# Kernel tuning notes

Measured on AMD Instinct MI355X. Metric: run time of the kernel, lower is better.

Reference implementation:

```python
import jax, jax.numpy as jnp
import numpy as np

N_NODES = 100_000
N_EDGES = 1_600_000
IN_CH, HID, OUT_CH = 2, 64, 16


def setup_inputs() -> dict:
    key = jax.random.key(0)
    ks = jax.random.split(key, 6)
    x = jax.random.normal(ks[0], (N_NODES, IN_CH), dtype=jnp.float32)
    edge_index = jax.random.randint(ks[1], (2, N_EDGES), 0, N_NODES, dtype=jnp.int64)
    # Glorot-style init for GCN weights
    W1 = jax.random.normal(ks[2], (IN_CH, HID), dtype=jnp.float32) / np.sqrt(IN_CH)
    b1 = jnp.zeros((HID,), dtype=jnp.float32)
    W_mu = jax.random.normal(ks[3], (HID, OUT_CH), dtype=jnp.float32) / np.sqrt(HID)
    b_mu = jnp.zeros((OUT_CH,), dtype=jnp.float32)
    W_logstd = jax.random.normal(ks[4], (HID, OUT_CH), dtype=jnp.float32) / np.sqrt(HID)
    b_logstd = jnp.zeros((OUT_CH,), dtype=jnp.float32)
    return dict(x=x, edge_index=edge_index, W1=W1, b1=b1,
                W_mu=W_mu, b_mu=b_mu, W_logstd=W_logstd, b_logstd=b_logstd)


def _gcn_conv(x, W, b, src, dst, deg_inv_sqrt, n):
    h = x @ W                                   # [n, out]
    norm = deg_inv_sqrt[src] * deg_inv_sqrt[dst]  # [E]
    agg = jax.ops.segment_sum(norm[:, None] * h[src], dst, num_segments=n)
    agg = agg + (deg_inv_sqrt * deg_inv_sqrt)[:, None] * h  # self-loop term
    return agg + b


def reference(x, edge_index, W1, b1, W_mu, b_mu, W_logstd, b_logstd):
    n = x.shape[0]
    src, dst = edge_index[0], edge_index[1]
    # degree on A+I (self-loop contributes 1)
    deg = 1.0 + jax.ops.segment_sum(jnp.ones_like(src, dtype=x.dtype), dst, num_segments=n)
    dis = jax.lax.rsqrt(deg)
    h = jax.nn.relu(_gcn_conv(x, W1, b1, src, dst, dis, n))
    mu = _gcn_conv(h, W_mu, b_mu, src, dst, dis, n)
    logstd = _gcn_conv(h, W_logstd, b_logstd, src, dst, dis, n)
    return (mu, logstd)
```

## Files before the change

kernel.cpp:

```cpp
#include <hip/hip_runtime.h>
#include <hip/hip_fp16.h>
#include <math.h>


#define CH    4096
#define CAPB  4800

typedef float f32x4 __attribute__((ext_vector_type(4)));

__device__ __forceinline__ float2 cvt2(unsigned u) {
    __half2 h = *reinterpret_cast<__half2*>(&u);
    return __half22float2(h);
}

__device__ __forceinline__ int block_scan512(int* arr, int* tmp, int tid) {
    int v0 = arr[2 * tid], v1 = arr[2 * tid + 1];
    tmp[tid] = v0 + v1;
    __syncthreads();
    for (int off = 1; off < 256; off <<= 1) {
        int a = (tid >= off) ? tmp[tid - off] : 0;
        __syncthreads();
        tmp[tid] += a;
        __syncthreads();
    }
    int incl = tmp[tid];
    int base = incl - v0 - v1;
    arr[2 * tid] = base;
    arr[2 * tid + 1] = base + v0;
    int total = tmp[255];
    __syncthreads();
    return total;
}

__global__ void k_chunksort(const int* __restrict__ src, const int* __restrict__ dst,
                            unsigned* __restrict__ pairsc, unsigned* __restrict__ seg_t,
                            int E, int NC, int NBk) {
    __shared__ int hist[512];
    __shared__ int tmp[256];
    __shared__ int cur[392];
    __shared__ unsigned ebuf[CH];
    int c = blockIdx.x, tid = threadIdx.x;
    int e0 = c * CH;
    int n_e = min(CH, E - e0);

    hist[tid] = 0; hist[tid + 256] = 0;
    __syncthreads();
    for (int i = tid; i < n_e; i += 256) {
        int d = dst[e0 + i];
        atomicAdd(&hist[d >> 8], 1);
    }
    __syncthreads();
    int total = block_scan512(hist, tmp, tid);
    cur[tid] = hist[tid];
    if (tid < 136) cur[tid + 256] = hist[tid + 256];
    __syncthreads();
    for (int i = tid; i < n_e; i += 256) {
        int d = dst[e0 + i];
        int s = src[e0 + i];
        int slot = atomicAdd(&cur[d >> 8], 1);
        ebuf[slot] = ((unsigned)(d & 255) << 17) | (unsigned)s;
    }
    __syncthreads();
    for (int i = tid; i < n_e; i += 256)
        pairsc[(size_t)e0 + i] = ebuf[i];
    for (int b = tid; b < NBk; b += 256) {
        int base = hist[b];
        int next = (b + 1 < 512) ? hist[b + 1] : total;
        seg_t[(size_t)b * NC + c] = ((unsigned)(next - base) << 13) | (unsigned)base;
    }
}

__global__ void k_bucket256(const unsigned* __restrict__ pairsc,
                            const unsigned* __restrict__ seg_t,
                            const float* __restrict__ x,
                            uint2* __restrict__ rows2, float2* __restrict__ xd,
                            int* __restrict__ sorted_src, int NC, int N) {
    __shared__ int coff[512];
    __shared__ int tmp[256];
    __shared__ int hist[512];
    __shared__ int cur[256];
    __shared__ unsigned segs[392];
    __shared__ unsigned lbuf[CAPB];
    __shared__ unsigned sbuf[CAPB];
    int b = blockIdx.x, tid = threadIdx.x;

    for (int c = tid; c < NC; c += 256) segs[c] = seg_t[(size_t)b * NC + c];
    coff[tid] = 0; coff[tid + 256] = 0;
    __syncthreads();
    for (int c = tid; c < NC; c += 256) coff[c] = (int)(segs[c] >> 13);
    __syncthreads();
    int tot = block_scan512(coff, tmp, tid);

    for (int c = tid; c < NC; c += 256) {
        unsigned sg = segs[c];
        int len = (int)(sg >> 13);
        int base = (int)(sg & 0x1FFFu);
        int doff = coff[c];
        const unsigned* p = pairsc + (size_t)c * CH + base;
        for (int j = 0; j < len; ++j) lbuf[doff + j] = p[j];
    }
    hist[tid] = 0; hist[tid + 256] = 0;
    __syncthreads();
    for (int i = tid; i < tot; i += 256) atomicAdd(&hist[lbuf[i] >> 17], 1);
    __syncthreads();
    int deg = hist[tid];
    block_scan512(hist, tmp, tid);
    int excl = hist[tid];
    int n = (b << 8) + tid;
    int ebase = b * CAPB;
    if (n < N) {
        float di = rsqrtf(1.0f + (float)deg);
        rows2[n] = make_uint2((unsigned)(ebase + excl) | ((unsigned)deg << 21),
                              __float_as_uint(di));
        float2 xv = ((const float2*)x)[n];
        xd[n] = make_float2(di * xv.x, di * xv.y);
    }
    cur[tid] = excl;
    __syncthreads();
    for (int i = tid; i < tot; i += 256) {
        unsigned pr = lbuf[i];
        int slot = atomicAdd(&cur[pr >> 17], 1);
        sbuf[slot] = pr & 0x1FFFFu;
    }
    __syncthreads();
    for (int i = tid; i < tot; i += 256)
        sorted_src[ebase + i] = (int)sbuf[i];
}

__global__ void k_mlp(const float2* __restrict__ xd, const uint2* __restrict__ rows2,
                      const int* __restrict__ sorted_src,
                      const float* __restrict__ W1, const float* __restrict__ b1,
                      const float* __restrict__ W_mu, const float* __restrict__ W_logstd,
                      __half2* __restrict__ hml16, int N) {
    __shared__ float2 Wp[64 * 16];
    int tid = threadIdx.x;
    for (int t = tid; t < 1024; t += 256) {
        int k = t >> 4, c2 = t & 15;
        Wp[t] = make_float2(W_mu[k * 16 + c2], W_logstd[k * 16 + c2]);
    }
    int c2 = tid & 15;
    float w1a[4], w1b[4], bb[4];
#pragma unroll
    for (int j = 0; j < 4; ++j) {
        w1a[j] = W1[c2 + 16 * j];
        w1b[j] = W1[64 + c2 + 16 * j];
        bb[j]  = b1[c2 + 16 * j];
    }
    __syncthreads();
    int node = blockIdx.x * 16 + (tid >> 4);
    if (node >= N) return;
    uint2 r = rows2[node];
    int beg = (int)(r.x & 0x1FFFFFu);
    int end = beg + (int)(r.x >> 21);
    float di = __uint_as_float(r.y);
    float sx = 0.0f, sy = 0.0f;
    for (int e = beg + c2; e < end; e += 16) {
        int s = sorted_src[e];
        float2 u = xd[s];
        sx += u.x;
        sy += u.y;
    }
#pragma unroll
    for (int off = 8; off; off >>= 1) {
        sx += __shfl_xor(sx, off, 16);
        sy += __shfl_xor(sy, off, 16);
    }
    float2 xn = xd[node];
    float axx = di * (sx + xn.x);
    float axy = di * (sy + xn.y);
    float h[4];
#pragma unroll
    for (int j = 0; j < 4; ++j)
        h[j] = fmaxf(fmaf(axx, w1a[j], fmaf(axy, w1b[j], bb[j])), 0.0f);
    float2 a0 = make_float2(0.f, 0.f), a1 = a0, a2 = a0, a3 = a0;
#pragma unroll
    for (int kk = 0; kk < 16; ++kk) {
        float h0 = __shfl(h[0], kk, 16);
        float h1 = __shfl(h[1], kk, 16);
        float h2 = __shfl(h[2], kk, 16);
        float h3 = __shfl(h[3], kk, 16);
        float2 w0 = Wp[kk * 16 + c2];
        float2 w1 = Wp[(16 + kk) * 16 + c2];
        float2 w2 = Wp[(32 + kk) * 16 + c2];
        float2 w3 = Wp[(48 + kk) * 16 + c2];
        a0.x = fmaf(h0, w0.x, a0.x); a0.y = fmaf(h0, w0.y, a0.y);
        a1.x = fmaf(h1, w1.x, a1.x); a1.y = fmaf(h1, w1.y, a1.y);
        a2.x = fmaf(h2, w2.x, a2.x); a2.y = fmaf(h2, w2.y, a2.y);
        a3.x = fmaf(h3, w3.x, a3.x); a3.y = fmaf(h3, w3.y, a3.y);
    }
    float mu = di * ((a0.x + a1.x) + (a2.x + a3.x));
    float ls = di * ((a0.y + a1.y) + (a2.y + a3.y));
    hml16[(size_t)node * 16 + c2] = __floats2half2_rn(mu, ls);
}

__global__ void k_agg2(const __half2* __restrict__ hml16, const uint2* __restrict__ rows2,
                       const int* __restrict__ sorted_src,
                       const float* __restrict__ b_mu, const float* __restrict__ b_logstd,
                       float* __restrict__ out, int N) {
    int t = blockIdx.x * blockDim.x + threadIdx.x;
    int node = t >> 2, q = t & 3;
    if (node >= N) return;
    const uint4* h4 = (const uint4*)hml16;
    uint2 r = rows2[node];
    int beg = (int)(r.x & 0x1FFFFFu);
    int end = beg + (int)(r.x >> 21);
    float di = __uint_as_float(r.y);
    uint4 v = h4[(size_t)node * 4 + q];
    float2 a0 = cvt2(v.x), a1 = cvt2(v.y), a2 = cvt2(v.z), a3 = cvt2(v.w);
    for (int k = beg; k < end; ++k) {
        int s = sorted_src[k];
        uint4 u = h4[(size_t)s * 4 + q];
        float2 t0 = cvt2(u.x), t1 = cvt2(u.y), t2 = cvt2(u.z), t3 = cvt2(u.w);
        a0.x += t0.x; a0.y += t0.y; a1.x += t1.x; a1.y += t1.y;
        a2.x += t2.x; a2.y += t2.y; a3.x += t3.x; a3.y += t3.y;
    }
    float4 bm = *(const float4*)(b_mu + 4 * q);
    float4 bl = *(const float4*)(b_logstd + 4 * q);
    f32x4 mu = { fmaf(di, a0.x, bm.x), fmaf(di, a1.x, bm.y),
                 fmaf(di, a2.x, bm.z), fmaf(di, a3.x, bm.w) };
    f32x4 ls = { fmaf(di, a0.y, bl.x), fmaf(di, a1.y, bl.y),
                 fmaf(di, a2.y, bl.z), fmaf(di, a3.y, bl.w) };
    *(f32x4*)(out + (size_t)node * 16 + 4 * q) = mu;
    *(f32x4*)(out + (size_t)(N + node) * 16 + 4 * q) = ls;
}

extern "C" void kernel_launch(void* const* d_in, const int* in_sizes, int n_in,
                              void* d_out, int out_size, void* d_ws, size_t ws_size,
                              hipStream_t stream) {
    const float* x        = (const float*)d_in[0];
    const int*   eidx     = (const int*)d_in[1];
    const float* W1       = (const float*)d_in[2];
    const float* b1       = (const float*)d_in[3];
    const float* W_mu     = (const float*)d_in[4];
    const float* b_mu     = (const float*)d_in[5];
    const float* W_logstd = (const float*)d_in[6];
    const float* b_logstd = (const float*)d_in[7];
    float* out = (float*)d_out;

    const int N = in_sizes[0] / 2;
    const int E = in_sizes[1] / 2;
    const int NC  = (E + CH - 1) / CH;
    const int NBk = (N + 255) >> 8;

    const int* src = eidx;
    const int* dst = eidx + E;

    char* w = (char*)d_ws;
    auto alloc = [&](size_t bytes) -> void* {
        void* p = (void*)w;
        w += (bytes + 255) & ~(size_t)255;
        return p;
    };
    unsigned* pairsc     = (unsigned*)alloc((size_t)NC * CH * 4);
    unsigned* seg_t      = (unsigned*)alloc((size_t)NBk * NC * 4);
    int*      sorted_src = (int*)     alloc((size_t)NBk * CAPB * 4);
    uint2*    rows2      = (uint2*)   alloc((size_t)N * 8);
    float2*   xd         = (float2*)  alloc((size_t)N * 8);
    __half2*  hml16      = (__half2*) alloc((size_t)N * 16 * 4);

    k_chunksort<<<NC, 256, 0, stream>>>(src, dst, pairsc, seg_t, E, NC, NBk);
    k_bucket256<<<NBk, 256, 0, stream>>>(pairsc, seg_t, x, rows2, xd,
                                         sorted_src, NC, N);
    k_mlp      <<<(N + 15) / 16, 256, 0, stream>>>(xd, rows2, sorted_src,
                                                   W1, b1, W_mu, W_logstd, hml16, N);
    k_agg2     <<<(4 * N + 255) / 256, 256, 0, stream>>>(hml16, rows2, sorted_src,
                                                         b_mu, b_logstd, out, N);
}
```

Baseline: 171.2 us.

## Assign one wavefront per node in final aggregation, splitting edges across sub-groups

```diff
diff --git a/kernel.cpp b/kernel.cpp
--- a/kernel.cpp
+++ b/kernel.cpp
@@ -193,35 +193,35 @@
     hml16[(size_t)node * 16 + c2] = __floats2half2_rn(mu, ls);
 }
 
-__global__ void k_agg2(const __half2* __restrict__ hml16, const uint2* __restrict__ rows2,
+__global__ void k_agg2(const unsigned* __restrict__ hml16u, const uint2* __restrict__ rows2,
                        const int* __restrict__ sorted_src,
                        const float* __restrict__ b_mu, const float* __restrict__ b_logstd,
                        float* __restrict__ out, int N) {
-    int t = blockIdx.x * blockDim.x + threadIdx.x;
-    int node = t >> 2, q = t & 3;
+    int node = blockIdx.x * 4 + (threadIdx.x >> 6);
     if (node >= N) return;
-    const uint4* h4 = (const uint4*)hml16;
+    int lane = threadIdx.x & 63;
+    int sub = lane >> 4;
+    int ch  = lane & 15;
     uint2 r = rows2[node];
     int beg = (int)(r.x & 0x1FFFFFu);
-    int end = beg + (int)(r.x >> 21);
+    int deg = (int)(r.x >> 21);
     float di = __uint_as_float(r.y);
-    uint4 v = h4[(size_t)node * 4 + q];
-    float2 a0 = cvt2(v.x), a1 = cvt2(v.y), a2 = cvt2(v.z), a3 = cvt2(v.w);
-    for (int k = beg; k < end; ++k) {
-        int s = sorted_src[k];
-        uint4 u = h4[(size_t)s * 4 + q];
-        float2 t0 = cvt2(u.x), t1 = cvt2(u.y), t2 = cvt2(u.z), t3 = cvt2(u.w);
-        a0.x += t0.x; a0.y += t0.y; a1.x += t1.x; a1.y += t1.y;
-        a2.x += t2.x; a2.y += t2.y; a3.x += t3.x; a3.y += t3.y;
-    }
-    float4 bm = *(const float4*)(b_mu + 4 * q);
-    float4 bl = *(const float4*)(b_logstd + 4 * q);
-    f32x4 mu = { fmaf(di, a0.x, bm.x), fmaf(di, a1.x, bm.y),
-                 fmaf(di, a2.x, bm.z), fmaf(di, a3.x, bm.w) };
-    f32x4 ls = { fmaf(di, a0.y, bl.x), fmaf(di, a1.y, bl.y),
-                 fmaf(di, a2.y, bl.z), fmaf(di, a3.y, bl.w) };
-    *(f32x4*)(out + (size_t)node * 16 + 4 * q) = mu;
-    *(f32x4*)(out + (size_t)(N + node) * 16 + 4 * q) = ls;
+    float2 acc = make_float2(0.0f, 0.0f);
+    if (sub == 0) acc = cvt2(hml16u[(size_t)node * 16 + ch]);
+    for (int k = sub; k < deg; k += 4) {
+        int s = sorted_src[beg + k];
+        float2 u = cvt2(hml16u[(size_t)s * 16 + ch]);
+        acc.x += u.x;
+        acc.y += u.y;
+    }
+    acc.x += __shfl_xor(acc.x, 16, 64);
+    acc.y += __shfl_xor(acc.y, 16, 64);
+    acc.x += __shfl_xor(acc.x, 32, 64);
+    acc.y += __shfl_xor(acc.y, 32, 64);
+    if (sub == 0) {
+        out[(size_t)node * 16 + ch]       = fmaf(di, acc.x, b_mu[ch]);
+        out[(size_t)(N + node) * 16 + ch] = fmaf(di, acc.y, b_logstd[ch]);
+    }
 }
 
 extern "C" void kernel_launch(void* const* d_in, const int* in_sizes, int n_in,
@@ -263,6 +263,6 @@
                                          sorted_src, NC, N);
     k_mlp      <<<(N + 15) / 16, 256, 0, stream>>>(xd, rows2, sorted_src,
                                                    W1, b1, W_mu, W_logstd, hml16, N);
-    k_agg2     <<<(4 * N + 255) / 256, 256, 0, stream>>>(hml16, rows2, sorted_src,
-                                                         b_mu, b_logstd, out, N);
-}
+    k_agg2     <<<(N + 3) / 4, 256, 0, stream>>>((const unsigned*)hml16, rows2,
+                                                 sorted_src, b_mu, b_logstd, out, N);
+}
```

Result: slower. 195.7 us (+14.3%).

## Sort nodes by degree within each bucket to balance wavefront work

Applied to the files above, without the earlier changes.

```diff
diff --git a/kernel.cpp b/kernel.cpp
--- a/kernel.cpp
+++ b/kernel.cpp
@@ -74,18 +74,22 @@
                             const unsigned* __restrict__ seg_t,
                             const float* __restrict__ x,
                             uint2* __restrict__ rows2, float2* __restrict__ xd,
-                            int* __restrict__ sorted_src, int NC, int N) {
+                            int* __restrict__ sorted_src, int* __restrict__ perm,
+                            int NC, int N) {
     __shared__ int coff[512];
     __shared__ int tmp[256];
     __shared__ int hist[512];
     __shared__ int cur[256];
     __shared__ unsigned segs[392];
+    __shared__ int hist2[64];
+    __shared__ int cur2[64];
     __shared__ unsigned lbuf[CAPB];
     __shared__ unsigned sbuf[CAPB];
     int b = blockIdx.x, tid = threadIdx.x;
 
     for (int c = tid; c < NC; c += 256) segs[c] = seg_t[(size_t)b * NC + c];
     coff[tid] = 0; coff[tid + 256] = 0;
+    if (tid < 64) hist2[tid] = 0;
     __syncthreads();
     for (int c = tid; c < NC; c += 256) coff[c] = (int)(segs[c] >> 13);
     __syncthreads();
@@ -115,8 +119,23 @@
         float2 xv = ((const float2*)x)[n];
         xd[n] = make_float2(di * xv.x, di * xv.y);
     }
+    int key = min(deg, 63);
+    atomicAdd(&hist2[key], 1);
     cur[tid] = excl;
     __syncthreads();
+    if (tid < 64) {
+        int v = hist2[tid];
+        int incl = v;
+        for (int off = 1; off < 64; off <<= 1) {
+            int a = __shfl_up(incl, off, 64);
+            if (tid >= off) incl += a;
+        }
+        cur2[tid] = incl - v;
+    }
+    __syncthreads();
+    int rank = atomicAdd(&cur2[key], 1);
+    perm[(b << 8) + rank] = n;
+
     for (int i = tid; i < tot; i += 256) {
         unsigned pr = lbuf[i];
         int slot = atomicAdd(&cur[pr >> 17], 1);
@@ -128,7 +147,7 @@
 }
 
 __global__ void k_mlp(const float2* __restrict__ xd, const uint2* __restrict__ rows2,
-                      const int* __restrict__ sorted_src,
+                      const int* __restrict__ sorted_src, const int* __restrict__ perm,
                       const float* __restrict__ W1, const float* __restrict__ b1,
                       const float* __restrict__ W_mu, const float* __restrict__ W_logstd,
                       __half2* __restrict__ hml16, int N) {
@@ -147,7 +166,7 @@
         bb[j]  = b1[c2 + 16 * j];
     }
     __syncthreads();
-    int node = blockIdx.x * 16 + (tid >> 4);
+    int node = perm[blockIdx.x * 16 + (tid >> 4)];
     if (node >= N) return;
     uint2 r = rows2[node];
     int beg = (int)(r.x & 0x1FFFFFu);
@@ -194,11 +213,12 @@
 }
 
 __global__ void k_agg2(const __half2* __restrict__ hml16, const uint2* __restrict__ rows2,
-                       const int* __restrict__ sorted_src,
+                       const int* __restrict__ sorted_src, const int* __restrict__ perm,
                        const float* __restrict__ b_mu, const float* __restrict__ b_logstd,
                        float* __restrict__ out, int N) {
     int t = blockIdx.x * blockDim.x + threadIdx.x;
-    int node = t >> 2, q = t & 3;
+    int node = perm[t >> 2];
+    int q = t & 3;
     if (node >= N) return;
     const uint4* h4 = (const uint4*)hml16;
     uint2 r = rows2[node];
@@ -241,6 +261,7 @@
     const int E = in_sizes[1] / 2;
     const int NC  = (E + CH - 1) / CH;
     const int NBk = (N + 255) >> 8;
+    const int SLOTS = NBk << 8;
 
     const int* src = eidx;
     const int* dst = eidx + E;
@@ -256,13 +277,14 @@
     int*      sorted_src = (int*)     alloc((size_t)NBk * CAPB * 4);
     uint2*    rows2      = (uint2*)   alloc((size_t)N * 8);
     float2*   xd         = (float2*)  alloc((size_t)N * 8);
+    int*      perm       = (int*)     alloc((size_t)SLOTS * 4);
     __half2*  hml16      = (__half2*) alloc((size_t)N * 16 * 4);
 
     k_chunksort<<<NC, 256, 0, stream>>>(src, dst, pairsc, seg_t, E, NC, NBk);
     k_bucket256<<<NBk, 256, 0, stream>>>(pairsc, seg_t, x, rows2, xd,
-                                         sorted_src, NC, N);
-    k_mlp      <<<(N + 15) / 16, 256, 0, stream>>>(xd, rows2, sorted_src,
-                                                   W1, b1, W_mu, W_logstd, hml16, N);
-    k_agg2     <<<(4 * N + 255) / 256, 256, 0, stream>>>(hml16, rows2, sorted_src,
-                                                         b_mu, b_logstd, out, N);
-}
+                                         sorted_src, perm, NC, N);
+    k_mlp      <<<SLOTS / 16, 256, 0, stream>>>(xd, rows2, sorted_src, perm,
+                                                W1, b1, W_mu, W_logstd, hml16, N);
+    k_agg2     <<<SLOTS * 4 / 256, 256, 0, stream>>>(hml16, rows2, sorted_src, perm,
+                                                     b_mu, b_logstd, out, N);
+}
```

New measurement: 180.1 us. +5.2%, slower.
